# Optimization experiments

Measured on AMD Instinct MI355X. Metric: run time of the kernel, lower is better.

Reference implementation:

```python
import jax, jax.numpy as jnp
import numpy as np
import math

N = 100000   # nodes
E = 1600000  # edges
H = 64       # hidden_dim
TD = 32      # time_dim
B = 8        # number of graphs in batch

def _lin(key, din, dout):
    kw, kb = jax.random.split(key)
    s = 1.0 / math.sqrt(din)
    return (jax.random.uniform(kw, (din, dout), jnp.float32, -s, s),
            jax.random.uniform(kb, (dout,), jnp.float32, -s, s))

def setup_inputs() -> dict:
    key = jax.random.key(0)
    ks = jax.random.split(key, 20)
    inp = {}
    inp['condition'] = jax.random.normal(ks[0], (N, 6), jnp.float32)
    inp['edge_attr'] = jax.random.normal(ks[1], (E, 2), jnp.float32)
    inp['edge_index'] = jax.random.randint(ks[2], (2, E), 0, N, jnp.int64 if jax.config.jax_enable_x64 else jnp.int32)
    inp['batch'] = jnp.sort(jax.random.randint(ks[3], (N,), 0, B))
    # node_mlp: 7->H->H
    inp['w_n1'], inp['b_n1'] = _lin(ks[4], 7, H)
    inp['w_n2'], inp['b_n2'] = _lin(ks[5], H, H)
    # edge_mlp: 2->H->H
    inp['w_e1'], inp['b_e1'] = _lin(ks[6], 2, H)
    inp['w_e2'], inp['b_e2'] = _lin(ks[7], H, H)
    # time_mlp: SiLU -> Linear(TD,H)
    inp['w_t'], inp['b_t'] = _lin(ks[8], TD, H)
    # three GINEConv inner MLPs: H->H->H each
    inp['w_c1a'], inp['b_c1a'] = _lin(ks[9], H, H)
    inp['w_c1b'], inp['b_c1b'] = _lin(ks[10], H, H)
    inp['w_c2a'], inp['b_c2a'] = _lin(ks[11], H, H)
    inp['w_c2b'], inp['b_c2b'] = _lin(ks[12], H, H)
    inp['w_c3a'], inp['b_c3a'] = _lin(ks[13], H, H)
    inp['w_c3b'], inp['b_c3b'] = _lin(ks[14], H, H)
    # final_mlp: H->H->1
    inp['w_f1'], inp['b_f1'] = _lin(ks[15], H, H)
    inp['w_f2'], inp['b_f2'] = _lin(ks[16], H, 1)
    return inp

def _mlp2(x, w1, b1, w2, b2):
    return jax.nn.silu(x @ w1 + b1) @ w2 + b2

def _time_emb(t, dim):
    half = dim // 2
    freqs = jnp.exp(jnp.arange(half, dtype=jnp.float32) * (-math.log(10000.0) / (half - 1)))
    ang = t[:, None].astype(jnp.float32) * freqs[None, :]
    return jnp.concatenate([jnp.sin(ang), jnp.cos(ang)], axis=-1)

def _gine_conv(h, ef, src, dst, w1, b1, w2, b2):
    # GINEConv (eps=0): nn(x_i + sum_j relu(x_j + edge_attr))
    msg = jax.nn.relu(h[src] + ef)                       # [E,H]
    agg = jax.ops.segment_sum(msg, dst, num_segments=N)  # [N,H]
    return _mlp2(h + agg, w1, b1, w2, b2)

def reference(condition, edge_attr,
              w_n1, b_n1, w_n2, b_n2,
              w_e1, b_e1, w_e2, b_e2,
              w_t, b_t,
              w_c1a, b_c1a, w_c1b, b_c1b,
              w_c2a, b_c2a, w_c2b, b_c2b,
              w_c3a, b_c3a, w_c3b, b_c3b,
              w_f1, b_f1, w_f2, b_f2,
              edge_index, batch):
    n = condition.shape[0]
    x_in = jnp.concatenate([jnp.zeros((n, 1), condition.dtype), condition], axis=-1)  # [N,7]
    h = _mlp2(x_in, w_n1, b_n1, w_n2, b_n2)          # [N,H]
    ef = _mlp2(edge_attr, w_e1, b_e1, w_e2, b_e2)    # [E,H]
    # t = zeros(batch_size) as in original; batch_size = B (static)
    t_emb = _time_emb(jnp.zeros((B,), jnp.float32), TD)   # [B,TD]
    t_feat = jax.nn.silu(t_emb) @ w_t + b_t               # [B,H]
    h = h + t_feat[batch]
    src, dst = edge_index[0], edge_index[1]
    h = jax.nn.silu(_gine_conv(h, ef, src, dst, w_c1a, b_c1a, w_c1b, b_c1b))
    h = jax.nn.silu(_gine_conv(h, ef, src, dst, w_c2a, b_c2a, w_c2b, b_c2b))
    h = jax.nn.silu(_gine_conv(h, ef, src, dst, w_c3a, b_c3a, w_c3b, b_c3b))
    return _mlp2(h, w_f1, b_f1, w_f2, b_f2)          # [N,1]
```

## Files before the change

### kernel.cpp

```cpp
#include <hip/hip_runtime.h>
#include <hip/hip_bf16.h>

#define NN 100000
#define NE 1600000
#define SCAN_BLOCKS 98

typedef short short8 __attribute__((ext_vector_type(8)));
typedef float floatx4 __attribute__((ext_vector_type(4)));
typedef int   intx4   __attribute__((ext_vector_type(4)));
typedef unsigned short ushortx4 __attribute__((ext_vector_type(4)));

__device__ __forceinline__ float silu_f(float x){ return x / (1.0f + __expf(-x)); }

__device__ __forceinline__ unsigned short f2bf(float x) {
    __hip_bfloat16 h = __float2bfloat16(x);
    unsigned short u; __builtin_memcpy(&u, &h, 2); return u;
}
__device__ __forceinline__ float bf2f(unsigned short u) {
    return __uint_as_float((unsigned)u << 16);
}

__device__ __forceinline__ float dot64(const float* vec, const float* wrow) {
    float ax = 0.f, ay = 0.f, az = 0.f, aw = 0.f;
#pragma unroll
    for (int k = 0; k < 64; k += 4) {
        float4 w = *(const float4*)(wrow + k);
        float4 v = *(const float4*)(vec + k);
        ax = fmaf(v.x, w.x, ax); ay = fmaf(v.y, w.y, ay);
        az = fmaf(v.z, w.z, az); aw = fmaf(v.w, w.w, aw);
    }
    return (ax + ay) + (az + aw);
}
__device__ __forceinline__ void load_wT(const float* __restrict__ w, float* s, int t) {
    for (int i = t; i < 4096; i += 256) { int k = i >> 6, j = i & 63; s[j * 68 + k] = w[i]; }
}

__global__ void tvec_kernel(const float* __restrict__ w_t, const float* __restrict__ b_t,
                            float* __restrict__ tvec) {
    int j = threadIdx.x;
    const float s1 = 0.7310585786300049f;
    float acc = b_t[j];
#pragma unroll
    for (int i = 16; i < 32; ++i) acc = fmaf(s1, w_t[i * 64 + j], acc);
    tvec[j] = acc;
}

__global__ __launch_bounds__(256) void node_init_kernel(
    const float* __restrict__ cond,
    const float* __restrict__ w1, const float* __restrict__ b1,
    const float* __restrict__ w2, const float* __restrict__ b2,
    const float* __restrict__ tvec,
    float* __restrict__ h, float* __restrict__ agg)
{
    __shared__ float s_w1[6 * 64];
    __shared__ float s_w2t[64 * 68];
    __shared__ float s_b1[64], s_b2[64];
    __shared__ float s_hid[4][64];
    int t = threadIdx.x;
    for (int i = t; i < 384; i += 256) s_w1[i] = w1[64 + i];
    load_wT(w2, s_w2t, t);
    if (t < 64) { s_b1[t] = b1[t]; s_b2[t] = b2[t] + tvec[t]; }
    __syncthreads();
    int lane = t & 63, grp = t >> 6;
    const int groups = (NN + 3) >> 2;
    for (int g = blockIdx.x; g < groups; g += gridDim.x) {
        int n = (g << 2) + grp;
        if (n < NN) {
            float acc = s_b1[lane];
#pragma unroll
            for (int i = 0; i < 6; ++i) acc = fmaf(cond[n * 6 + i], s_w1[i * 64 + lane], acc);
            s_hid[grp][lane] = silu_f(acc);
            float o = s_b2[lane] + dot64(s_hid[grp], s_w2t + lane * 68);
            size_t off = (size_t)n * 64 + lane;
            h[off] = o;
            if (agg) agg[off] = 0.f;
        }
    }
}

__global__ __launch_bounds__(256) void zero_kernel(int* __restrict__ p, int n) {
    int i = blockIdx.x * 256 + threadIdx.x;
    if (i < n) p[i] = 0;
}
__global__ __launch_bounds__(256) void hist_rank_kernel(const int* __restrict__ dst,
                                                        int* __restrict__ cnt,
                                                        int* __restrict__ rank) {
    int e = blockIdx.x * 256 + threadIdx.x;
    if (e < NE) rank[e] = atomicAdd(&cnt[dst[e]], 1);
}
__global__ __launch_bounds__(256) void scan1_kernel(const int* __restrict__ cnt,
                                                    int* __restrict__ offs, int* __restrict__ bsum) {
    __shared__ int s_w[4];
    int t = threadIdx.x;
    int base = blockIdx.x * 1024 + t * 4;
    int v0 = (base + 0 < NN) ? cnt[base + 0] : 0;
    int v1 = (base + 1 < NN) ? cnt[base + 1] : 0;
    int v2 = (base + 2 < NN) ? cnt[base + 2] : 0;
    int v3 = (base + 3 < NN) ? cnt[base + 3] : 0;
    int tsum = v0 + v1 + v2 + v3;
    int lane = t & 63, w = t >> 6;
    int x = tsum;
#pragma unroll
    for (int d = 1; d < 64; d <<= 1) { int y = __shfl_up(x, d, 64); if (lane >= d) x += y; }
    if (lane == 63) s_w[w] = x;
    __syncthreads();
    if (t == 0) {
        int a = 0;
#pragma unroll
        for (int i = 0; i < 4; ++i) { int b = s_w[i]; s_w[i] = a; a += b; }
        bsum[blockIdx.x] = a;
    }
    __syncthreads();
    int excl = x - tsum + s_w[w];
    if (base + 0 < NN) offs[base + 0] = excl;
    if (base + 1 < NN) offs[base + 1] = excl + v0;
    if (base + 2 < NN) offs[base + 2] = excl + v0 + v1;
    if (base + 3 < NN) offs[base + 3] = excl + v0 + v1 + v2;
}
__global__ void scan2_kernel(const int* __restrict__ bsum, int* __restrict__ bscan, int nb) {
    __shared__ int s_w[2];
    int t = threadIdx.x;
    int v = (t < nb) ? bsum[t] : 0;
    int lane = t & 63, w = t >> 6;
    int x = v;
#pragma unroll
    for (int d = 1; d < 64; d <<= 1) { int y = __shfl_up(x, d, 64); if (lane >= d) x += y; }
    if (lane == 63) s_w[w] = x;
    __syncthreads();
    int add = (w == 1) ? s_w[0] : 0;
    if (t < nb) bscan[t] = x - v + add;
}
__global__ __launch_bounds__(256) void scan3_kernel(int* __restrict__ offs,
                                                    const int* __restrict__ bscan) {
    int i = blockIdx.x * 256 + threadIdx.x;
    if (i < NN) offs[i] = offs[i] + bscan[i >> 10];
    if (i == 0) offs[NN] = NE;
}
__global__ __launch_bounds__(256) void scatter_pack_kernel(const int* __restrict__ dst,
                                                           const int* __restrict__ src,
                                                           const float* __restrict__ ea,
                                                           const int* __restrict__ offs,
                                                           const int* __restrict__ rank,
                                                           intx4* __restrict__ pack) {
    int e = blockIdx.x * 256 + threadIdx.x;
    if (e >= NE) return;
    float2 a = *(const float2*)(ea + (size_t)e * 2);
    int pos = offs[dst[e]] + rank[e];
    intx4 p = { src[e], __float_as_int(a.x), __float_as_int(a.y), 0 };
    pack[pos] = p;
}
__global__ __launch_bounds__(256) void copy_src_kernel(const intx4* __restrict__ pack,
                                                       int* __restrict__ srcc) {
    int i = blockIdx.x * 256 + threadIdx.x;
    if (i < NE) srcc[i] = pack[i].x;
}

__global__ __launch_bounds__(256, 2) void edge_feat_mfma_kernel(
    const intx4* __restrict__ pack,
    const float* __restrict__ w1, const float* __restrict__ b1,
    const float* __restrict__ w2, const float* __restrict__ b2,
    __hip_bfloat16* __restrict__ ef)
{
    int t = threadIdx.x;
    int lane = t & 63, wv = t >> 6;
    int er = lane & 15;
    int kg = lane >> 4;
    float w1x[2][8], w1y[2][8], b1v[2][8];
#pragma unroll
    for (int c = 0; c < 2; ++c)
#pragma unroll
        for (int j = 0; j < 8; ++j) {
            int k = c * 32 + kg * 8 + j;
            w1x[c][j] = w1[k];
            w1y[c][j] = w1[64 + k];
            b1v[c][j] = b1[k];
        }
    short8 bfrag[2][4];
#pragma unroll
    for (int c = 0; c < 2; ++c)
#pragma unroll
        for (int tt = 0; tt < 4; ++tt)
#pragma unroll
            for (int j = 0; j < 8; ++j) {
                int k = c * 32 + kg * 8 + j;
                bfrag[c][tt][j] = (short)f2bf(w2[k * 64 + 4 * er + tt]);
            }
    float4 b2v = *(const float4*)(b2 + 4 * er);

    const int nchunk = NE / 16;
    for (int ch = blockIdx.x * 4 + wv; ch < nchunk; ch += gridDim.x * 4) {
        int i0 = ch * 16;
        intx4 p = __builtin_nontemporal_load(pack + i0 + er);
        float ax = __int_as_float(p.y), ay = __int_as_float(p.z);
        short8 afrag[2];
#pragma unroll
        for (int c = 0; c < 2; ++c)
#pragma unroll
            for (int j = 0; j < 8; ++j) {
                float hid = silu_f(fmaf(ax, w1x[c][j], fmaf(ay, w1y[c][j], b1v[c][j])));
                afrag[c][j] = (short)f2bf(hid);
            }
        floatx4 acc0 = {0,0,0,0}, acc1 = {0,0,0,0}, acc2 = {0,0,0,0}, acc3 = {0,0,0,0};
        acc0 = __builtin_amdgcn_mfma_f32_16x16x32_bf16(afrag[0], bfrag[0][0], acc0, 0, 0, 0);
        acc0 = __builtin_amdgcn_mfma_f32_16x16x32_bf16(afrag[1], bfrag[1][0], acc0, 0, 0, 0);
        acc1 = __builtin_amdgcn_mfma_f32_16x16x32_bf16(afrag[0], bfrag[0][1], acc1, 0, 0, 0);
        acc1 = __builtin_amdgcn_mfma_f32_16x16x32_bf16(afrag[1], bfrag[1][1], acc1, 0, 0, 0);
        acc2 = __builtin_amdgcn_mfma_f32_16x16x32_bf16(afrag[0], bfrag[0][2], acc2, 0, 0, 0);
        acc2 = __builtin_amdgcn_mfma_f32_16x16x32_bf16(afrag[1], bfrag[1][2], acc2, 0, 0, 0);
        acc3 = __builtin_amdgcn_mfma_f32_16x16x32_bf16(afrag[0], bfrag[0][3], acc3, 0, 0, 0);
        acc3 = __builtin_amdgcn_mfma_f32_16x16x32_bf16(afrag[1], bfrag[1][3], acc3, 0, 0, 0);
#pragma unroll
        for (int q = 0; q < 4; ++q) {
            ushortx4 o;
            o.x = f2bf(acc0[q] + b2v.x);
            o.y = f2bf(acc1[q] + b2v.y);
            o.z = f2bf(acc2[q] + b2v.z);
            o.w = f2bf(acc3[q] + b2v.w);
            __builtin_nontemporal_store(o,
                (ushortx4*)((unsigned short*)ef + (size_t)(i0 + kg * 4 + q) * 64 + 4 * er));
        }
    }
}

__global__ __launch_bounds__(256) void agg_kernel(
    const float* __restrict__ hin, float* __restrict__ u,
    const int* __restrict__ offs, const int* __restrict__ srcc,
    const __hip_bfloat16* __restrict__ ef)
{
    int t = threadIdx.x;
    int lane = t & 63, wv = t >> 6;
    int half = lane >> 5, l32 = lane & 31;
    int n = blockIdx.x * 8 + wv * 2 + half;
    if (n >= NN) return;
    size_t off = (size_t)n * 64 + l32 * 2;
    float2 acc = *(const float2*)(hin + off);
    const unsigned int* efu = (const unsigned int*)ef;
    int i0 = offs[n], i1 = offs[n + 1];
    for (int ib = i0; ib < i1; ib += 32) {
        int m = i1 - ib; if (m > 32) m = 32;
        int myS = 0;
        if (l32 < m) myS = __builtin_nontemporal_load(srcc + ib + l32);
        int j = 0;
        for (; j + 8 <= m; j += 8) {
            float2 hs[8]; unsigned int ev[8];
#pragma unroll
            for (int q = 0; q < 8; ++q) {
                int s = __shfl(myS, j + q, 32);
                hs[q] = *(const float2*)(hin + (size_t)s * 64 + l32 * 2);
                ev[q] = __builtin_nontemporal_load(efu + (size_t)(ib + j + q) * 32 + l32);
            }
#pragma unroll
            for (int q = 0; q < 8; ++q) {
                acc.x += fmaxf(hs[q].x + bf2f((unsigned short)(ev[q] & 0xffffu)), 0.f);
                acc.y += fmaxf(hs[q].y + bf2f((unsigned short)(ev[q] >> 16)), 0.f);
            }
        }
        for (; j < m; ++j) {
            int s = __shfl(myS, j, 32);
            float2 hs = *(const float2*)(hin + (size_t)s * 64 + l32 * 2);
            unsigned int ev = __builtin_nontemporal_load(efu + (size_t)(ib + j) * 32 + l32);
            acc.x += fmaxf(hs.x + bf2f((unsigned short)(ev & 0xffffu)), 0.f);
            acc.y += fmaxf(hs.y + bf2f((unsigned short)(ev >> 16)), 0.f);
        }
    }
    *(float2*)(u + off) = acc;
}

__global__ __launch_bounds__(256) void node_mlp_mfma_kernel(
    const float* __restrict__ u, float* __restrict__ h,
    const float* __restrict__ wa, const float* __restrict__ ba,
    const float* __restrict__ wb, const float* __restrict__ bb)
{
    __shared__ float s_hid[4][16 * 72];
    int t = threadIdx.x, lane = t & 63, wv = t >> 6;
    int er = lane & 15, kg = lane >> 4;
    short8 waH[2][4], waL[2][4], wbH[2][4], wbL[2][4];
#pragma unroll
    for (int c = 0; c < 2; ++c)
#pragma unroll
        for (int tt = 0; tt < 4; ++tt)
#pragma unroll
            for (int j = 0; j < 8; ++j) {
                int k = c * 32 + kg * 8 + j;
                float vA = wa[k * 64 + 4 * er + tt];
                unsigned short hA = f2bf(vA);
                waH[c][tt][j] = (short)hA;
                waL[c][tt][j] = (short)f2bf(vA - bf2f(hA));
                float vB = wb[k * 64 + 4 * er + tt];
                unsigned short hB = f2bf(vB);
                wbH[c][tt][j] = (short)hB;
                wbL[c][tt][j] = (short)f2bf(vB - bf2f(hB));
            }
    float4 bav = *(const float4*)(ba + 4 * er);
    float4 bbv = *(const float4*)(bb + 4 * er);
    float* hid = s_hid[wv];

    const int ntile = NN / 16;
    for (int tile = blockIdx.x * 4 + wv; tile < ntile; tile += gridDim.x * 4) {
        int i0 = tile * 16;
        short8 aH[2], aL[2];
#pragma unroll
        for (int c = 0; c < 2; ++c) {
            const float* up = u + (size_t)(i0 + er) * 64 + c * 32 + kg * 8;
            float4 u0 = *(const float4*)(up);
            float4 u1 = *(const float4*)(up + 4);
            float uv[8] = {u0.x, u0.y, u0.z, u0.w, u1.x, u1.y, u1.z, u1.w};
#pragma unroll
            for (int j = 0; j < 8; ++j) {
                unsigned short hi = f2bf(uv[j]);
                aH[c][j] = (short)hi;
                aL[c][j] = (short)f2bf(uv[j] - bf2f(hi));
            }
        }
        floatx4 acc[4] = {{0,0,0,0},{0,0,0,0},{0,0,0,0},{0,0,0,0}};
#pragma unroll
        for (int tt = 0; tt < 4; ++tt)
#pragma unroll
            for (int c = 0; c < 2; ++c) {
                acc[tt] = __builtin_amdgcn_mfma_f32_16x16x32_bf16(aH[c], waH[c][tt], acc[tt], 0, 0, 0);
                acc[tt] = __builtin_amdgcn_mfma_f32_16x16x32_bf16(aL[c], waH[c][tt], acc[tt], 0, 0, 0);
                acc[tt] = __builtin_amdgcn_mfma_f32_16x16x32_bf16(aH[c], waL[c][tt], acc[tt], 0, 0, 0);
            }
#pragma unroll
        for (int q = 0; q < 4; ++q) {
            float4 hv;
            hv.x = silu_f(acc[0][q] + bav.x);
            hv.y = silu_f(acc[1][q] + bav.y);
            hv.z = silu_f(acc[2][q] + bav.z);
            hv.w = silu_f(acc[3][q] + bav.w);
            *(float4*)(hid + (kg * 4 + q) * 72 + 4 * er) = hv;
        }
        short8 cH[2], cL[2];
#pragma unroll
        for (int c = 0; c < 2; ++c) {
            const float* hp = hid + er * 72 + c * 32 + kg * 8;
            float4 h0 = *(const float4*)(hp);
            float4 h1 = *(const float4*)(hp + 4);
            float hv[8] = {h0.x, h0.y, h0.z, h0.w, h1.x, h1.y, h1.z, h1.w};
#pragma unroll
            for (int j = 0; j < 8; ++j) {
                unsigned short hi = f2bf(hv[j]);
                cH[c][j] = (short)hi;
                cL[c][j] = (short)f2bf(hv[j] - bf2f(hi));
            }
        }
        floatx4 acc2[4] = {{0,0,0,0},{0,0,0,0},{0,0,0,0},{0,0,0,0}};
#pragma unroll
        for (int tt = 0; tt < 4; ++tt)
#pragma unroll
            for (int c = 0; c < 2; ++c) {
                acc2[tt] = __builtin_amdgcn_mfma_f32_16x16x32_bf16(cH[c], wbH[c][tt], acc2[tt], 0, 0, 0);
                acc2[tt] = __builtin_amdgcn_mfma_f32_16x16x32_bf16(cL[c], wbH[c][tt], acc2[tt], 0, 0, 0);
                acc2[tt] = __builtin_amdgcn_mfma_f32_16x16x32_bf16(cH[c], wbL[c][tt], acc2[tt], 0, 0, 0);
            }
#pragma unroll
        for (int q = 0; q < 4; ++q) {
            float4 ov;
            ov.x = silu_f(acc2[0][q] + bbv.x);
            ov.y = silu_f(acc2[1][q] + bbv.y);
            ov.z = silu_f(acc2[2][q] + bbv.z);
            ov.w = silu_f(acc2[3][q] + bbv.w);
            *(float4*)(h + (size_t)(i0 + kg * 4 + q) * 64 + 4 * er) = ov;
        }
    }
}

__global__ __launch_bounds__(256, 3) void edge_feat_fallback_kernel(
    const float* __restrict__ ea,
    const float* __restrict__ w1, const float* __restrict__ b1,
    const float* __restrict__ w2, const float* __restrict__ b2,
    __hip_bfloat16* __restrict__ ef)
{
    __shared__ float s_w1[128], s_b1[64], s_b2[64];
    __shared__ float s_hid[4][64];
    int t = threadIdx.x;
    if (t < 128) s_w1[t] = w1[t];
    if (t < 64) { s_b1[t] = b1[t]; s_b2[t] = b2[t]; }
    int lane = t & 63, grp = t >> 6;
    __syncthreads();
    const int groups = NE >> 2;
    for (int g = blockIdx.x; g < groups; g += gridDim.x) {
        int e = (g << 2) + grp;
        float2 a = *(const float2*)(ea + (size_t)e * 2);
        float acc = fmaf(a.x, s_w1[lane], fmaf(a.y, s_w1[64 + lane], s_b1[lane]));
        s_hid[grp][lane] = silu_f(acc);
        float o = s_b2[lane];
#pragma unroll
        for (int k = 0; k < 64; k += 4) {
            float4 v = *(const float4*)&s_hid[grp][k];
            o = fmaf(v.x, w2[(k+0)*64+lane], o);
            o = fmaf(v.y, w2[(k+1)*64+lane], o);
            o = fmaf(v.z, w2[(k+2)*64+lane], o);
            o = fmaf(v.w, w2[(k+3)*64+lane], o);
        }
        ef[(size_t)e * 64 + lane] = __float2bfloat16(o);
    }
}

__global__ __launch_bounds__(256) void msg_agg_kernel(
    const int* __restrict__ src, const int* __restrict__ dst,
    const float* __restrict__ h, const __hip_bfloat16* __restrict__ ef,
    float* __restrict__ agg)
{
    int tid = blockIdx.x * 256 + threadIdx.x;
    int e = tid >> 4;
    if (e >= NE) return;
    int q = tid & 15;
    int s = src[e], d = dst[e];
    float4 hv = *(const float4*)(h + (size_t)s * 64 + q * 4);
    ushort4 ev = *(const ushort4*)(ef + (size_t)e * 64 + q * 4);
    float m0 = fmaxf(hv.x + __uint_as_float((unsigned)ev.x << 16), 0.f);
    float m1 = fmaxf(hv.y + __uint_as_float((unsigned)ev.y << 16), 0.f);
    float m2 = fmaxf(hv.z + __uint_as_float((unsigned)ev.z << 16), 0.f);
    float m3 = fmaxf(hv.w + __uint_as_float((unsigned)ev.w << 16), 0.f);
    float* ap = agg + (size_t)d * 64 + q * 4;
    atomicAdd(ap + 0, m0); atomicAdd(ap + 1, m1);
    atomicAdd(ap + 2, m2); atomicAdd(ap + 3, m3);
}

__global__ __launch_bounds__(256) void node_update_kernel(
    float* __restrict__ h, float* __restrict__ agg,
    const float* __restrict__ wa, const float* __restrict__ ba,
    const float* __restrict__ wb, const float* __restrict__ bb)
{
    __shared__ float s_wat[64 * 68], s_wbt[64 * 68];
    __shared__ float s_ba[64], s_bb[64];
    __shared__ float s_u[4][64], s_hid[4][64];
    int t = threadIdx.x;
    load_wT(wa, s_wat, t);
    load_wT(wb, s_wbt, t);
    if (t < 64) { s_ba[t] = ba[t]; s_bb[t] = bb[t]; }
    __syncthreads();
    int lane = t & 63, grp = t >> 6;
    const int groups = (NN + 3) >> 2;
    for (int g = blockIdx.x; g < groups; g += gridDim.x) {
        int n = (g << 2) + grp;
        if (n < NN) {
            size_t off = (size_t)n * 64 + lane;
            float uv = h[off] + agg[off];
            agg[off] = 0.f;
            s_u[grp][lane] = uv;
            float hid = silu_f(s_ba[lane] + dot64(s_u[grp], s_wat + lane * 68));
            s_hid[grp][lane] = hid;
            float o = silu_f(s_bb[lane] + dot64(s_hid[grp], s_wbt + lane * 68));
            h[off] = o;
        }
    }
}

__global__ __launch_bounds__(256) void final_kernel(
    const float* __restrict__ hin,
    const float* __restrict__ w1, const float* __restrict__ b1,
    const float* __restrict__ w2, const float* __restrict__ b2,
    float* __restrict__ out)
{
    __shared__ float s_w1t[64 * 68];
    __shared__ float s_b1[64], s_w2[64];
    __shared__ float s_u[4][64];
    int t = threadIdx.x;
    load_wT(w1, s_w1t, t);
    if (t < 64) { s_b1[t] = b1[t]; s_w2[t] = w2[t]; }
    __syncthreads();
    int lane = t & 63, grp = t >> 6;
    float b2v = b2[0];
    const int groups = (NN + 3) >> 2;
    for (int g = blockIdx.x; g < groups; g += gridDim.x) {
        int n = (g << 2) + grp;
        if (n < NN) {
            s_u[grp][lane] = hin[(size_t)n * 64 + lane];
            float hid = silu_f(s_b1[lane] + dot64(s_u[grp], s_w1t + lane * 68));
            float v = hid * s_w2[lane];
#pragma unroll
            for (int off = 32; off; off >>= 1) v += __shfl_xor(v, off, 64);
            if (lane == 0) out[n] = v + b2v;
        }
    }
}

extern "C" void kernel_launch(void* const* d_in, const int* in_sizes, int n_in,
                              void* d_out, int out_size, void* d_ws, size_t ws_size,
                              hipStream_t stream) {
    const float* cond = (const float*)d_in[0];
    const float* ea   = (const float*)d_in[1];
    const int*   ei   = (const int*)d_in[2];
    const float* w_n1 = (const float*)d_in[4];  const float* b_n1 = (const float*)d_in[5];
    const float* w_n2 = (const float*)d_in[6];  const float* b_n2 = (const float*)d_in[7];
    const float* w_e1 = (const float*)d_in[8];  const float* b_e1 = (const float*)d_in[9];
    const float* w_e2 = (const float*)d_in[10]; const float* b_e2 = (const float*)d_in[11];
    const float* w_t  = (const float*)d_in[12]; const float* b_t  = (const float*)d_in[13];
    const float* wca[3] = {(const float*)d_in[14], (const float*)d_in[18], (const float*)d_in[22]};
    const float* bca[3] = {(const float*)d_in[15], (const float*)d_in[19], (const float*)d_in[23]};
    const float* wcb[3] = {(const float*)d_in[16], (const float*)d_in[20], (const float*)d_in[24]};
    const float* bcb[3] = {(const float*)d_in[17], (const float*)d_in[21], (const float*)d_in[25]};
    const float* w_f1 = (const float*)d_in[26]; const float* b_f1 = (const float*)d_in[27];
    const float* w_f2 = (const float*)d_in[28]; const float* b_f2 = (const float*)d_in[29];
    float* out = (float*)d_out;

    const int* srcp = ei;
    const int* dstp = ei + NE;
    char* ws = (char*)d_ws;

    size_t o = 0;
    float* tvec = (float*)(ws + o); o += 256;
    float* h    = (float*)(ws + o); o += (size_t)NN * 64 * 4;
    float* u    = (float*)(ws + o); o += (size_t)NN * 64 * 4;
    int* offs   = (int*)(ws + o);   o += ((size_t)(NN + 1) * 4 + 255) & ~255ULL;
    int* cnt    = (int*)(ws + o);   o += ((size_t)NN * 4 + 255) & ~255ULL;
    int* bsum   = (int*)(ws + o);   o += 512;
    int* bscan  = (int*)(ws + o);   o += 512;
    int* srcc   = (int*)(ws + o);   o += (size_t)NE * 4;
    __hip_bfloat16* ef = (__hip_bfloat16*)(ws + o); o += (size_t)NE * 64 * 2;
    const size_t REQ_A = o;
    intx4* pack = (intx4*)u;
    int* rank = srcc;

    if (ws_size >= REQ_A) {
        hipLaunchKernelGGL(tvec_kernel, dim3(1), dim3(64), 0, stream, w_t, b_t, tvec);
        hipLaunchKernelGGL(zero_kernel, dim3((NN + 255) / 256), dim3(256), 0, stream, cnt, NN);
        hipLaunchKernelGGL(hist_rank_kernel, dim3((NE + 255) / 256), dim3(256), 0, stream,
                           dstp, cnt, rank);
        hipLaunchKernelGGL(scan1_kernel, dim3(SCAN_BLOCKS), dim3(256), 0, stream, cnt, offs, bsum);
        hipLaunchKernelGGL(scan2_kernel, dim3(1), dim3(128), 0, stream, bsum, bscan, SCAN_BLOCKS);
        hipLaunchKernelGGL(scan3_kernel, dim3((NN + 255) / 256), dim3(256), 0, stream, offs, bscan);
        hipLaunchKernelGGL(scatter_pack_kernel, dim3((NE + 255) / 256), dim3(256), 0, stream,
                           dstp, srcp, ea, offs, rank, pack);
        hipLaunchKernelGGL(copy_src_kernel, dim3((NE + 255) / 256), dim3(256), 0, stream,
                           pack, srcc);
        hipLaunchKernelGGL(node_init_kernel, dim3(1024), dim3(256), 0, stream,
                           cond, w_n1, b_n1, w_n2, b_n2, tvec, h, (float*)nullptr);
        hipLaunchKernelGGL(edge_feat_mfma_kernel, dim3(2048), dim3(256), 0, stream,
                           pack, w_e1, b_e1, w_e2, b_e2, ef);
        for (int l = 0; l < 3; ++l) {
            hipLaunchKernelGGL(agg_kernel, dim3((NN + 7) / 8), dim3(256), 0, stream,
                               h, u, offs, srcc, ef);
            hipLaunchKernelGGL(node_mlp_mfma_kernel, dim3(391), dim3(256), 0, stream,
                               u, h, wca[l], bca[l], wcb[l], bcb[l]);
        }
        hipLaunchKernelGGL(final_kernel, dim3(1024), dim3(256), 0, stream,
                           h, w_f1, b_f1, w_f2, b_f2, out);
    } else {
        float* tvecB = (float*)ws;
        float* hB    = (float*)(ws + 256);
        float* agg   = hB + (size_t)NN * 64;
        __hip_bfloat16* efB = (__hip_bfloat16*)(agg + (size_t)NN * 64);
        hipLaunchKernelGGL(tvec_kernel, dim3(1), dim3(64), 0, stream, w_t, b_t, tvecB);
        hipLaunchKernelGGL(node_init_kernel, dim3(1024), dim3(256), 0, stream,
                           cond, w_n1, b_n1, w_n2, b_n2, tvecB, hB, agg);
        hipLaunchKernelGGL(edge_feat_fallback_kernel, dim3(1024), dim3(256), 0, stream,
                           ea, w_e1, b_e1, w_e2, b_e2, efB);
        for (int l = 0; l < 3; ++l) {
            hipLaunchKernelGGL(msg_agg_kernel, dim3((NE * 16) / 256), dim3(256), 0, stream,
                               srcp, dstp, hB, efB, agg);
            hipLaunchKernelGGL(node_update_kernel, dim3(1024), dim3(256), 0, stream,
                               hB, agg, wca[l], bca[l], wcb[l], bcb[l]);
        }
        hipLaunchKernelGGL(final_kernel, dim3(1024), dim3(256), 0, stream,
                           hB, w_f1, b_f1, w_f2, b_f2, out);
    }
}
```

Baseline: 580.3 us.

## Fuse edge MLP into aggregation, recomputing edge features per layer

Removes the materialized bf16 edge-feature buffer (1.6M x 64) and the copy_src pass. Each aggregation layer now recomputes the edge MLP with MFMA from the packed edge attributes and accumulates relu(h[src]+ef) directly. The aim is to stop writing and re-reading about 200 MB of edge features per layer, at the cost of redoing the edge MLP compute three times. It also switches to one node per wavefront with 16-edge chunks, which leaves many lanes idle for low-degree nodes, and adds padding of the pack buffer.

```diff
diff --git a/kernel.cpp b/kernel.cpp
--- a/kernel.cpp
+++ b/kernel.cpp
@@ -8,7 +8,6 @@
 typedef short short8 __attribute__((ext_vector_type(8)));
 typedef float floatx4 __attribute__((ext_vector_type(4)));
 typedef int   intx4   __attribute__((ext_vector_type(4)));
-typedef unsigned short ushortx4 __attribute__((ext_vector_type(4)));
 
 __device__ __forceinline__ float silu_f(float x){ return x / (1.0f + __expf(-x)); }
 
@@ -149,22 +148,19 @@
     intx4 p = { src[e], __float_as_int(a.x), __float_as_int(a.y), 0 };
     pack[pos] = p;
 }
-__global__ __launch_bounds__(256) void copy_src_kernel(const intx4* __restrict__ pack,
-                                                       int* __restrict__ srcc) {
-    int i = blockIdx.x * 256 + threadIdx.x;
-    if (i < NE) srcc[i] = pack[i].x;
-}
-
-__global__ __launch_bounds__(256, 2) void edge_feat_mfma_kernel(
-    const intx4* __restrict__ pack,
+__global__ void pad_pack_kernel(intx4* __restrict__ pack) {
+    intx4 z = {0, 0, 0, 0};
+    pack[NE + threadIdx.x] = z;
+}
+
+__global__ __launch_bounds__(256, 2) void agg_fused_kernel(
+    const float* __restrict__ hin, float* __restrict__ u,
+    const int* __restrict__ offs, const intx4* __restrict__ pack,
     const float* __restrict__ w1, const float* __restrict__ b1,
-    const float* __restrict__ w2, const float* __restrict__ b2,
-    __hip_bfloat16* __restrict__ ef)
-{
-    int t = threadIdx.x;
-    int lane = t & 63, wv = t >> 6;
-    int er = lane & 15;
-    int kg = lane >> 4;
+    const float* __restrict__ w2, const float* __restrict__ b2)
+{
+    int t = threadIdx.x, lane = t & 63, wv = t >> 6;
+    int er = lane & 15, kg = lane >> 4;
     float w1x[2][8], w1y[2][8], b1v[2][8];
 #pragma unroll
     for (int c = 0; c < 2; ++c)
@@ -187,83 +183,58 @@
             }
     float4 b2v = *(const float4*)(b2 + 4 * er);
 
-    const int nchunk = NE / 16;
-    for (int ch = blockIdx.x * 4 + wv; ch < nchunk; ch += gridDim.x * 4) {
-        int i0 = ch * 16;
-        intx4 p = __builtin_nontemporal_load(pack + i0 + er);
-        float ax = __int_as_float(p.y), ay = __int_as_float(p.z);
+    int n = blockIdx.x * 4 + wv;
+    if (n >= NN) return;
+    int i0 = offs[n], i1 = offs[n + 1];
+    float ax0 = 0.f, ax1 = 0.f, ax2 = 0.f, ax3 = 0.f;
+    for (int ib = i0; ib < i1; ib += 16) {
+        int m = i1 - ib; if (m > 16) m = 16;
+        intx4 p = pack[ib + er];
+        float eax = __int_as_float(p.y), eay = __int_as_float(p.z);
         short8 afrag[2];
 #pragma unroll
         for (int c = 0; c < 2; ++c)
 #pragma unroll
             for (int j = 0; j < 8; ++j) {
-                float hid = silu_f(fmaf(ax, w1x[c][j], fmaf(ay, w1y[c][j], b1v[c][j])));
+                float hid = silu_f(fmaf(eax, w1x[c][j], fmaf(eay, w1y[c][j], b1v[c][j])));
                 afrag[c][j] = (short)f2bf(hid);
             }
-        floatx4 acc0 = {0,0,0,0}, acc1 = {0,0,0,0}, acc2 = {0,0,0,0}, acc3 = {0,0,0,0};
-        acc0 = __builtin_amdgcn_mfma_f32_16x16x32_bf16(afrag[0], bfrag[0][0], acc0, 0, 0, 0);
-        acc0 = __builtin_amdgcn_mfma_f32_16x16x32_bf16(afrag[1], bfrag[1][0], acc0, 0, 0, 0);
-        acc1 = __builtin_amdgcn_mfma_f32_16x16x32_bf16(afrag[0], bfrag[0][1], acc1, 0, 0, 0);
-        acc1 = __builtin_amdgcn_mfma_f32_16x16x32_bf16(afrag[1], bfrag[1][1], acc1, 0, 0, 0);
-        acc2 = __builtin_amdgcn_mfma_f32_16x16x32_bf16(afrag[0], bfrag[0][2], acc2, 0, 0, 0);
-        acc2 = __builtin_amdgcn_mfma_f32_16x16x32_bf16(afrag[1], bfrag[1][2], acc2, 0, 0, 0);
-        acc3 = __builtin_amdgcn_mfma_f32_16x16x32_bf16(afrag[0], bfrag[0][3], acc3, 0, 0, 0);
-        acc3 = __builtin_amdgcn_mfma_f32_16x16x32_bf16(afrag[1], bfrag[1][3], acc3, 0, 0, 0);
+        floatx4 e0 = {0,0,0,0}, e1 = {0,0,0,0}, e2 = {0,0,0,0}, e3 = {0,0,0,0};
+        e0 = __builtin_amdgcn_mfma_f32_16x16x32_bf16(afrag[0], bfrag[0][0], e0, 0, 0, 0);
+        e0 = __builtin_amdgcn_mfma_f32_16x16x32_bf16(afrag[1], bfrag[1][0], e0, 0, 0, 0);
+        e1 = __builtin_amdgcn_mfma_f32_16x16x32_bf16(afrag[0], bfrag[0][1], e1, 0, 0, 0);
+        e1 = __builtin_amdgcn_mfma_f32_16x16x32_bf16(afrag[1], bfrag[1][1], e1, 0, 0, 0);
+        e2 = __builtin_amdgcn_mfma_f32_16x16x32_bf16(afrag[0], bfrag[0][2], e2, 0, 0, 0);
+        e2 = __builtin_amdgcn_mfma_f32_16x16x32_bf16(afrag[1], bfrag[1][2], e2, 0, 0, 0);
+        e3 = __builtin_amdgcn_mfma_f32_16x16x32_bf16(afrag[0], bfrag[0][3], e3, 0, 0, 0);
+        e3 = __builtin_amdgcn_mfma_f32_16x16x32_bf16(afrag[1], bfrag[1][3], e3, 0, 0, 0);
 #pragma unroll
         for (int q = 0; q < 4; ++q) {
-            ushortx4 o;
-            o.x = f2bf(acc0[q] + b2v.x);
-            o.y = f2bf(acc1[q] + b2v.y);
-            o.z = f2bf(acc2[q] + b2v.z);
-            o.w = f2bf(acc3[q] + b2v.w);
-            __builtin_nontemporal_store(o,
-                (ushortx4*)((unsigned short*)ef + (size_t)(i0 + kg * 4 + q) * 64 + 4 * er));
-        }
-    }
-}
-
-__global__ __launch_bounds__(256) void agg_kernel(
-    const float* __restrict__ hin, float* __restrict__ u,
-    const int* __restrict__ offs, const int* __restrict__ srcc,
-    const __hip_bfloat16* __restrict__ ef)
-{
-    int t = threadIdx.x;
-    int lane = t & 63, wv = t >> 6;
-    int half = lane >> 5, l32 = lane & 31;
-    int n = blockIdx.x * 8 + wv * 2 + half;
-    if (n >= NN) return;
-    size_t off = (size_t)n * 64 + l32 * 2;
-    float2 acc = *(const float2*)(hin + off);
-    const unsigned int* efu = (const unsigned int*)ef;
-    int i0 = offs[n], i1 = offs[n + 1];
-    for (int ib = i0; ib < i1; ib += 32) {
-        int m = i1 - ib; if (m > 32) m = 32;
-        int myS = 0;
-        if (l32 < m) myS = __builtin_nontemporal_load(srcc + ib + l32);
-        int j = 0;
-        for (; j + 8 <= m; j += 8) {
-            float2 hs[8]; unsigned int ev[8];
-#pragma unroll
-            for (int q = 0; q < 8; ++q) {
-                int s = __shfl(myS, j + q, 32);
-                hs[q] = *(const float2*)(hin + (size_t)s * 64 + l32 * 2);
-                ev[q] = __builtin_nontemporal_load(efu + (size_t)(ib + j + q) * 32 + l32);
-            }
-#pragma unroll
-            for (int q = 0; q < 8; ++q) {
-                acc.x += fmaxf(hs[q].x + bf2f((unsigned short)(ev[q] & 0xffffu)), 0.f);
-                acc.y += fmaxf(hs[q].y + bf2f((unsigned short)(ev[q] >> 16)), 0.f);
-            }
-        }
-        for (; j < m; ++j) {
-            int s = __shfl(myS, j, 32);
-            float2 hs = *(const float2*)(hin + (size_t)s * 64 + l32 * 2);
-            unsigned int ev = __builtin_nontemporal_load(efu + (size_t)(ib + j) * 32 + l32);
-            acc.x += fmaxf(hs.x + bf2f((unsigned short)(ev & 0xffffu)), 0.f);
-            acc.y += fmaxf(hs.y + bf2f((unsigned short)(ev >> 16)), 0.f);
-        }
-    }
-    *(float2*)(u + off) = acc;
+            int r = kg * 4 + q;
+            int sr = __shfl(p.x, r, 64);
+            if (r < m) {
+                float4 hv = *(const float4*)(hin + (size_t)sr * 64 + 4 * er);
+                ax0 += fmaxf(hv.x + e0[q] + b2v.x, 0.f);
+                ax1 += fmaxf(hv.y + e1[q] + b2v.y, 0.f);
+                ax2 += fmaxf(hv.z + e2[q] + b2v.z, 0.f);
+                ax3 += fmaxf(hv.w + e3[q] + b2v.w, 0.f);
+            }
+        }
+    }
+#pragma unroll
+    for (int d = 16; d <= 32; d <<= 1) {
+        ax0 += __shfl_xor(ax0, d, 64);
+        ax1 += __shfl_xor(ax1, d, 64);
+        ax2 += __shfl_xor(ax2, d, 64);
+        ax3 += __shfl_xor(ax3, d, 64);
+    }
+    if (kg == 0) {
+        float4 self = *(const float4*)(hin + (size_t)n * 64 + 4 * er);
+        float4 o;
+        o.x = self.x + ax0; o.y = self.y + ax1;
+        o.z = self.z + ax2; o.w = self.w + ax3;
+        *(float4*)(u + (size_t)n * 64 + 4 * er) = o;
+    }
 }
 
 __global__ __launch_bounds__(256) void node_mlp_mfma_kernel(
@@ -508,11 +479,9 @@
     int* cnt    = (int*)(ws + o);   o += ((size_t)NN * 4 + 255) & ~255ULL;
     int* bsum   = (int*)(ws + o);   o += 512;
     int* bscan  = (int*)(ws + o);   o += 512;
-    int* srcc   = (int*)(ws + o);   o += (size_t)NE * 4;
-    __hip_bfloat16* ef = (__hip_bfloat16*)(ws + o); o += (size_t)NE * 64 * 2;
+    int* rank   = (int*)(ws + o);   o += (size_t)NE * 4;
+    intx4* pack = (intx4*)(ws + o); o += (size_t)(NE + 16) * 16;
     const size_t REQ_A = o;
-    intx4* pack = (intx4*)u;
-    int* rank = srcc;
 
     if (ws_size >= REQ_A) {
         hipLaunchKernelGGL(tvec_kernel, dim3(1), dim3(64), 0, stream, w_t, b_t, tvec);
@@ -524,15 +493,12 @@
         hipLaunchKernelGGL(scan3_kernel, dim3((NN + 255) / 256), dim3(256), 0, stream, offs, bscan);
         hipLaunchKernelGGL(scatter_pack_kernel, dim3((NE + 255) / 256), dim3(256), 0, stream,
                            dstp, srcp, ea, offs, rank, pack);
-        hipLaunchKernelGGL(copy_src_kernel, dim3((NE + 255) / 256), dim3(256), 0, stream,
-                           pack, srcc);
+        hipLaunchKernelGGL(pad_pack_kernel, dim3(1), dim3(16), 0, stream, pack);
         hipLaunchKernelGGL(node_init_kernel, dim3(1024), dim3(256), 0, stream,
                            cond, w_n1, b_n1, w_n2, b_n2, tvec, h, (float*)nullptr);
-        hipLaunchKernelGGL(edge_feat_mfma_kernel, dim3(2048), dim3(256), 0, stream,
-                           pack, w_e1, b_e1, w_e2, b_e2, ef);
         for (int l = 0; l < 3; ++l) {
-            hipLaunchKernelGGL(agg_kernel, dim3((NN + 7) / 8), dim3(256), 0, stream,
-                               h, u, offs, srcc, ef);
+            hipLaunchKernelGGL(agg_fused_kernel, dim3((NN + 3) / 4), dim3(256), 0, stream,
+                               h, u, offs, pack, w_e1, b_e1, w_e2, b_e2);
             hipLaunchKernelGGL(node_mlp_mfma_kernel, dim3(391), dim3(256), 0, stream,
                                u, h, wca[l], bca[l], wcb[l], bcb[l]);
         }
```

Result: slower. 897.7 us (+54.7%).

## Process four edges per half-wave with 16-byte loads in aggregation

Applied to the files above, without the earlier changes.

Restructures the GINE aggregation so each 32-lane half-wave handles four edges at once: 8 lanes per edge each load 16 bytes of bf16 edge features and 32 bytes of the source row, with 8 per-lane accumulators reduced by xor-shuffles at the end. This replaces the per-edge 4/8-byte loads with wider vector loads and fewer loop iterations, aiming to raise memory-level parallelism on the gather. Out-of-range lanes in a partial group read padding, so the edge-feature buffer is extended by four rows. It adds a cross-lane reduction and leaves some lanes idle on the tail edges.

```diff
diff --git a/kernel.cpp b/kernel.cpp
--- a/kernel.cpp
+++ b/kernel.cpp
@@ -8,6 +8,7 @@
 typedef short short8 __attribute__((ext_vector_type(8)));
 typedef float floatx4 __attribute__((ext_vector_type(4)));
 typedef int   intx4   __attribute__((ext_vector_type(4)));
+typedef unsigned int uintx4 __attribute__((ext_vector_type(4)));
 typedef unsigned short ushortx4 __attribute__((ext_vector_type(4)));
 
 __device__ __forceinline__ float silu_f(float x){ return x / (1.0f + __expf(-x)); }
@@ -19,6 +20,8 @@
 __device__ __forceinline__ float bf2f(unsigned short u) {
     return __uint_as_float((unsigned)u << 16);
 }
+__device__ __forceinline__ float bflo(unsigned int v) { return __uint_as_float(v << 16); }
+__device__ __forceinline__ float bfhi(unsigned int v) { return __uint_as_float(v & 0xffff0000u); }
 
 __device__ __forceinline__ float dot64(const float* vec, const float* wrow) {
     float ax = 0.f, ay = 0.f, az = 0.f, aw = 0.f;
@@ -230,40 +233,53 @@
     int t = threadIdx.x;
     int lane = t & 63, wv = t >> 6;
     int half = lane >> 5, l32 = lane & 31;
+    int c = l32 & 7, rs = l32 >> 3;
     int n = blockIdx.x * 8 + wv * 2 + half;
     if (n >= NN) return;
-    size_t off = (size_t)n * 64 + l32 * 2;
-    float2 acc = *(const float2*)(hin + off);
     const unsigned int* efu = (const unsigned int*)ef;
     int i0 = offs[n], i1 = offs[n + 1];
+    float a0 = 0.f, a1 = 0.f, a2 = 0.f, a3 = 0.f, a4 = 0.f, a5 = 0.f, a6 = 0.f, a7 = 0.f;
     for (int ib = i0; ib < i1; ib += 32) {
         int m = i1 - ib; if (m > 32) m = 32;
         int myS = 0;
         if (l32 < m) myS = __builtin_nontemporal_load(srcc + ib + l32);
-        int j = 0;
-        for (; j + 8 <= m; j += 8) {
-            float2 hs[8]; unsigned int ev[8];
-#pragma unroll
-            for (int q = 0; q < 8; ++q) {
-                int s = __shfl(myS, j + q, 32);
-                hs[q] = *(const float2*)(hin + (size_t)s * 64 + l32 * 2);
-                ev[q] = __builtin_nontemporal_load(efu + (size_t)(ib + j + q) * 32 + l32);
-            }
-#pragma unroll
-            for (int q = 0; q < 8; ++q) {
-                acc.x += fmaxf(hs[q].x + bf2f((unsigned short)(ev[q] & 0xffffu)), 0.f);
-                acc.y += fmaxf(hs[q].y + bf2f((unsigned short)(ev[q] >> 16)), 0.f);
-            }
-        }
-        for (; j < m; ++j) {
-            int s = __shfl(myS, j, 32);
-            float2 hs = *(const float2*)(hin + (size_t)s * 64 + l32 * 2);
-            unsigned int ev = __builtin_nontemporal_load(efu + (size_t)(ib + j) * 32 + l32);
-            acc.x += fmaxf(hs.x + bf2f((unsigned short)(ev & 0xffffu)), 0.f);
-            acc.y += fmaxf(hs.y + bf2f((unsigned short)(ev >> 16)), 0.f);
-        }
-    }
-    *(float2*)(u + off) = acc;
+        for (int rb = 0; rb < m; rb += 4) {
+            int r = rb + rs;
+            int s = __shfl(myS, r, 32);
+            bool valid = r < m;
+            if (!valid) s = 0;
+            uintx4 ev = __builtin_nontemporal_load(
+                (const uintx4*)(efu + (size_t)(ib + r) * 32 + c * 4));
+            float4 h0 = *(const float4*)(hin + (size_t)s * 64 + c * 8);
+            float4 h1 = *(const float4*)(hin + (size_t)s * 64 + c * 8 + 4);
+            if (valid) {
+                a0 += fmaxf(h0.x + bflo(ev.x), 0.f);
+                a1 += fmaxf(h0.y + bfhi(ev.x), 0.f);
+                a2 += fmaxf(h0.z + bflo(ev.y), 0.f);
+                a3 += fmaxf(h0.w + bfhi(ev.y), 0.f);
+                a4 += fmaxf(h1.x + bflo(ev.z), 0.f);
+                a5 += fmaxf(h1.y + bfhi(ev.z), 0.f);
+                a6 += fmaxf(h1.z + bflo(ev.w), 0.f);
+                a7 += fmaxf(h1.w + bfhi(ev.w), 0.f);
+            }
+        }
+    }
+#pragma unroll
+    for (int d = 8; d <= 16; d <<= 1) {
+        a0 += __shfl_xor(a0, d, 32); a1 += __shfl_xor(a1, d, 32);
+        a2 += __shfl_xor(a2, d, 32); a3 += __shfl_xor(a3, d, 32);
+        a4 += __shfl_xor(a4, d, 32); a5 += __shfl_xor(a5, d, 32);
+        a6 += __shfl_xor(a6, d, 32); a7 += __shfl_xor(a7, d, 32);
+    }
+    if (rs == 0) {
+        float4 s0 = *(const float4*)(hin + (size_t)n * 64 + c * 8);
+        float4 s1 = *(const float4*)(hin + (size_t)n * 64 + c * 8 + 4);
+        float4 o0, o1;
+        o0.x = s0.x + a0; o0.y = s0.y + a1; o0.z = s0.z + a2; o0.w = s0.w + a3;
+        o1.x = s1.x + a4; o1.y = s1.y + a5; o1.z = s1.z + a6; o1.w = s1.w + a7;
+        *(float4*)(u + (size_t)n * 64 + c * 8) = o0;
+        *(float4*)(u + (size_t)n * 64 + c * 8 + 4) = o1;
+    }
 }
 
 __global__ __launch_bounds__(256) void node_mlp_mfma_kernel(
@@ -509,7 +525,7 @@
     int* bsum   = (int*)(ws + o);   o += 512;
     int* bscan  = (int*)(ws + o);   o += 512;
     int* srcc   = (int*)(ws + o);   o += (size_t)NE * 4;
-    __hip_bfloat16* ef = (__hip_bfloat16*)(ws + o); o += (size_t)NE * 64 * 2;
+    __hip_bfloat16* ef = (__hip_bfloat16*)(ws + o); o += (size_t)(NE + 4) * 64 * 2;
     const size_t REQ_A = o;
     intx4* pack = (intx4*)u;
     int* rank = srcc;
```

Measured after the change: 577.9 us (median of 2 runs). About the same (-0.4%).
